# Optimization experiments

Hardware: AMD Instinct MI355X
Metric: run time of the kernel (lower is better)

Reference implementation:

```python
import jax, jax.numpy as jnp
import numpy as np

GROUPS = 32
EPS = 1e-5


def _group_norm(x, scale, bias):
    B, C, H, W = x.shape
    xg = x.reshape(B, GROUPS, -1)
    mu = xg.mean(axis=-1, keepdims=True)
    var = jnp.mean(jnp.square(xg - mu), axis=-1, keepdims=True)
    xn = ((xg - mu) * jax.lax.rsqrt(var + EPS)).reshape(B, C, H, W)
    return xn * scale[None, :, None, None] + bias[None, :, None, None]


def _conv1x1(x, w, b):
    # x: [B,C,H,W], w: [O,C], b: [O]
    return jnp.einsum('bchw,oc->bohw', x, w) + b[None, :, None, None]


def setup_inputs() -> dict:
    key = jax.random.key(0)
    ks = jax.random.split(key, 6)
    B, C, H, W = 16, 512, 32, 32
    x = jax.random.normal(ks[0], (B, C, H, W), dtype=jnp.float32)
    # xavier_uniform for [C, C, 1, 1] conv: limit = sqrt(6 / (fan_in + fan_out)) = sqrt(6 / (2C))
    lim = float(np.sqrt(6.0 / (2 * C)))
    wq = jax.random.uniform(ks[1], (C, C), jnp.float32, -lim, lim)
    wk = jax.random.uniform(ks[2], (C, C), jnp.float32, -lim, lim)
    wv = jax.random.uniform(ks[3], (C, C), jnp.float32, -lim, lim)
    wo = jax.random.uniform(ks[4], (C, C), jnp.float32, -lim, lim) * 1e-5  # gain=1e-5
    zeros_c = jnp.zeros((C,), jnp.float32)
    return {
        'x': x,
        'gn_scale': jnp.ones((C,), jnp.float32),
        'gn_bias': zeros_c,
        'wq': wq, 'bq': zeros_c,
        'wk': wk, 'bk': zeros_c,
        'wv': wv, 'bv': zeros_c,
        'wo': wo, 'bo': zeros_c,
    }


def reference(x, gn_scale, gn_bias, wq, bq, wk, bk, wv, bv, wo, bo):
    B, C, H, W = x.shape
    N = H * W
    h = _group_norm(x, gn_scale, gn_bias)
    q = _conv1x1(h, wq, bq).reshape(B, C, N)  # [B,C,N]
    k = _conv1x1(h, wk, bk).reshape(B, C, N)
    v = _conv1x1(h, wv, bv).reshape(B, C, N)
    scale = 1.0 / jnp.sqrt(jnp.asarray(C, x.dtype))
    w = jnp.einsum('bcn,bcm->bnm', q, k) * scale  # [B,N,N]
    w = jax.nn.softmax(w, axis=-1)
    hv = jnp.einsum('bnm,bcm->bcn', w, v).reshape(B, C, H, W)
    out = _conv1x1(hv, wo, bo)
    return x + out
```

## Files before the change

kernel.cpp:

```cpp
#include <hip/hip_runtime.h>
#include <hip/hip_bf16.h>
#include <cstdint>

typedef unsigned char u8;
typedef float floatx4 __attribute__((ext_vector_type(4)));
typedef int intx8 __attribute__((ext_vector_type(8)));

__device__ __forceinline__ void gld_lds16(const void* g, void* l) {
    __builtin_amdgcn_global_load_lds(
        (const __attribute__((address_space(1))) unsigned int*)g,
        (__attribute__((address_space(3))) unsigned int*)l, 16, 0, 0);
}

__device__ __forceinline__ u8 f2fp8(float v) {
    return (u8)(__builtin_amdgcn_cvt_pk_fp8_f32(v, v, 0, false) & 0xff);
}
__device__ __forceinline__ unsigned int pack4_fp8(float a, float b, float c, float d) {
    unsigned int u = __builtin_amdgcn_cvt_pk_fp8_f32(a, b, 0, false);
    u = __builtin_amdgcn_cvt_pk_fp8_f32(c, d, u, true);
    return u;
}

__device__ __forceinline__ intx8 ld_frag(const u8* p, int lo, int hi) {
    uint4 a = *(const uint4*)(p + lo);
    uint4 b = *(const uint4*)(p + hi);
    intx8 r;
    r[0] = a.x; r[1] = a.y; r[2] = a.z; r[3] = a.w;
    r[4] = b.x; r[5] = b.y; r[6] = b.z; r[7] = b.w;
    return r;
}
__device__ __forceinline__ intx8 ld_frag_g(const u8* p) {
    uint4 a = *(const uint4*)(p);
    uint4 b = *(const uint4*)(p + 16);
    intx8 r;
    r[0] = a.x; r[1] = a.y; r[2] = a.z; r[3] = a.w;
    r[4] = b.x; r[5] = b.y; r[6] = b.z; r[7] = b.w;
    return r;
}


__global__ __launch_bounds__(256) void setup_kernel(
    const float* __restrict__ x, const float* __restrict__ gs,
    const float* __restrict__ gb,
    const float* __restrict__ wq, const float* __restrict__ wk,
    const float* __restrict__ wv, const float* __restrict__ wo,
    const float* __restrict__ bq, const float* __restrict__ bk,
    const float* __restrict__ bv,
    u8* __restrict__ hT, u8* __restrict__ wqkv, u8* __restrict__ wob,
    float* __restrict__ bqkv)
{
    const int t = threadIdx.x;
    if (blockIdx.x >= 512) {
        int i = (blockIdx.x - 512) * 256 + t;
        if (i < 786432) {
            int which = i >> 18;
            int off = i & 262143;
            const float* src = which == 0 ? wq : which == 1 ? wk : wv;
            wqkv[i] = f2fp8(src[off]);
        } else {
            int i2 = i - 786432;
            int row = i2 >> 9, col = i2 & 511;
            wob[(long long)(row >> 4) * 8192 + (col >> 5) * 512
                + (row & 15) * 32 + (col & 31)] = f2fp8(wo[i2] * 262144.0f);
        }
        if (i < 1536)
            bqkv[i] = i < 512 ? bq[i] : (i < 1024 ? bk[i - 512] : bv[i - 1024]);
        return;
    }
    const int b = blockIdx.x >> 5;
    const int g = blockIdx.x & 31;
    const int wave = t >> 6, lane = t & 63;
    const float4* x4 = (const float4*)(x + ((long long)b * 512 + g * 16) * 1024);

    float4 v[16];
    float s1 = 0.f, s2 = 0.f;
#pragma unroll
    for (int i = 0; i < 16; ++i) {
        v[i] = x4[i * 256 + t];
        s1 += v[i].x + v[i].y + v[i].z + v[i].w;
        s2 += v[i].x * v[i].x + v[i].y * v[i].y + v[i].z * v[i].z + v[i].w * v[i].w;
    }
#pragma unroll
    for (int m = 32; m; m >>= 1) {
        s1 += __shfl_xor(s1, m, 64);
        s2 += __shfl_xor(s2, m, 64);
    }
    __shared__ float red[2][4];
    __shared__ float stats[2];
    if (lane == 0) { red[0][wave] = s1; red[1][wave] = s2; }
    __syncthreads();
    if (t == 0) {
        float a = red[0][0] + red[0][1] + red[0][2] + red[0][3];
        float q = red[1][0] + red[1][1] + red[1][2] + red[1][3];
        float mu = a * (1.0f / 16384.0f);
        float var = q * (1.0f / 16384.0f) - mu * mu;
        stats[0] = mu;
        stats[1] = rsqrtf(var + 1e-5f);
    }
    __syncthreads();
    const float mu = stats[0], rs = stats[1];

#pragma unroll
    for (int i = 0; i < 16; ++i) {
        const float sc = gs[g * 16 + i] * rs;
        const float bi = gb[g * 16 + i] - mu * sc;
        v[i].x = v[i].x * sc + bi;
        v[i].y = v[i].y * sc + bi;
        v[i].z = v[i].z * sc + bi;
        v[i].w = v[i].w * sc + bi;
    }
    u8* hb = hT + (long long)b * 524288 + g * 16;
#pragma unroll
    for (int r = 0; r < 4; ++r) {
        uint4 o;
        o.x = pack4_fp8(v[0][r],  v[1][r],  v[2][r],  v[3][r]);
        o.y = pack4_fp8(v[4][r],  v[5][r],  v[6][r],  v[7][r]);
        o.z = pack4_fp8(v[8][r],  v[9][r],  v[10][r], v[11][r]);
        o.w = pack4_fp8(v[12][r], v[13][r], v[14][r], v[15][r]);
        *(uint4*)(hb + (long long)(4 * t + r) * 512) = o;
    }
}

template <int EPI>
__global__ __launch_bounds__(256, 3) void gemm_mx(
    const u8* __restrict__ A, long long sA,
    const u8* __restrict__ B, long long sB,
    void* __restrict__ C, long long sC,
    void* __restrict__ C2, void* __restrict__ C3,
    int ldC, int K,
    const float* __restrict__ bias)
{
    __shared__ __align__(16) u8 smem[33792];
    const int tid = threadIdx.x;
    const int l = tid & 63;
    const int wave = tid >> 6;
    const int wm = wave >> 1, wn = wave & 1;
    const int bm = blockIdx.x, bn = blockIdx.y, b = blockIdx.z;

    const u8* Ab = A + (long long)b * sA + (long long)bm * 128 * K;
    const u8* Bb = B + (long long)b * sB + (long long)bn * 128 * K;

    const int srow = wave * 8 + (l >> 3);
    const int sg = ((l & 7) ^ ((l >> 3) & 7)) * 16;
    const u8* ga  = Ab + (long long)srow * K + sg;
    const u8* gbp = Bb + (long long)srow * K + sg;
    const long long c32 = (long long)32 * K;
    const int ldst = wave * 1024;

    const int q4 = l >> 4;
    const int ln = l & 15;
    const int glo = ((2 * q4) ^ (l & 7)) * 16;
    const int ghi = ((2 * q4 + 1) ^ (l & 7)) * 16;
    int arow[4], brow[4];
#pragma unroll
    for (int i = 0; i < 4; ++i) {
        arow[i] = (wm * 64 + i * 16 + ln) * 128;
        brow[i] = (wn * 64 + i * 16 + ln) * 128 + 16384;
    }

    floatx4 acc[4][4] = {};
    const int niter = K >> 7;

    for (int it = 0; it < niter; ++it) {
        const int k0 = it << 7;
#pragma unroll
        for (int c = 0; c < 4; ++c) {
            gld_lds16(ga + c * c32 + k0, smem + c * 4096 + ldst);
            gld_lds16(gbp + c * c32 + k0, smem + 16384 + c * 4096 + ldst);
        }
        __syncthreads();
        intx8 bfr[4];
#pragma unroll
        for (int j = 0; j < 4; ++j) bfr[j] = ld_frag(smem + brow[j], glo, ghi);
#pragma unroll
        for (int i = 0; i < 4; ++i) {
            intx8 af = ld_frag(smem + arow[i], glo, ghi);
#pragma unroll
            for (int j = 0; j < 4; ++j)
                acc[i][j] = __builtin_amdgcn_mfma_scale_f32_16x16x128_f8f6f4(
                    af, bfr[j], acc[i][j], 0, 0, 0, 127, 0, 127);
        }
        __syncthreads();
    }

    {
        const int which = bn >> 2;
        u8* tile = smem;
#pragma unroll
        for (int i = 0; i < 4; ++i) {
            const int rl = wm * 64 + i * 16 + q4 * 4;
#pragma unroll
            for (int j = 0; j < 4; ++j) {
                const int cl = wn * 64 + j * 16 + ln;
                const float badd = bias[bn * 128 + cl];
                if (which == 2) {
                    *(unsigned int*)(tile + cl * 144 + rl) =
                        pack4_fp8(acc[i][j][0] + badd, acc[i][j][1] + badd,
                                  acc[i][j][2] + badd, acc[i][j][3] + badd);
                } else {
#pragma unroll
                    for (int r = 0; r < 4; ++r)
                        tile[(rl + r) * 144 + cl] = f2fp8(acc[i][j][r] + badd);
                }
            }
        }
        __syncthreads();
        const int w2  = wave >> 1;
        const int cbl = (wave & 1) * 2 + (l >> 5);
        const int lnw = (l >> 1) & 15;
        const int g16 = (l & 1) * 16;
#pragma unroll
        for (int p = 0; p < 4; ++p) {
            const int rtile = p * 2 + w2;
            uint4 dd = *(const uint4*)(tile + (rtile * 16 + lnw) * 144 + cbl * 32 + g16);
            u8* dst;
            if (which == 0)
                dst = (u8*)C + (long long)b * sC + (long long)(bm * 8 + rtile) * 8192
                      + ((bn & 3) * 4 + cbl) * 512 + lnw * 32 + g16;
            else if (which == 1)
                dst = (u8*)C2 + (long long)b * sC + (long long)(bm * 8 + rtile) * 8192
                      + ((bn & 3) * 4 + cbl) * 512 + lnw * 32 + g16;
            else
                dst = (u8*)C3 + (long long)b * sC + (long long)((bn & 3) * 8 + rtile) * 16384
                      + (long long)(bm * 4 + cbl) * 512 + lnw * 32 + g16;
            *(uint4*)dst = dd;
        }
    }
}

__global__ __launch_bounds__(256, 2) void attn_out(
    const u8* __restrict__ qg, const u8* __restrict__ kg,
    const u8* __restrict__ vg, const u8* __restrict__ wot,
    const float* __restrict__ bo, const float* __restrict__ xg,
    float* __restrict__ outg)
{
    __shared__ __align__(16) u8 smem[25088];
    const int tid = threadIdx.x;
    const int l = tid & 63;
    const int w = tid >> 6;
    const int d = blockIdx.x;
    const int b  = (d & 7) * 2 + ((d >> 8) & 1);
    const int bq = (d >> 3) & 31;

    const u8* qb = qg + (long long)b * 524288 + (long long)(bq * 2) * 8192;
    const u8* kb = kg + (long long)b * 524288;
    const u8* vb = vg + (long long)b * 524288;

    const int q4 = l >> 4;
    const int ln = l & 15;
    const int glo = ((2 * q4) ^ (l & 7)) * 16;
    const int ghi = ((2 * q4 + 1) ^ (l & 7)) * 16;
    const int lo32 = ln * 32;

    intx8 qf[2][4];
#pragma unroll
    for (int j = 0; j < 2; ++j)
#pragma unroll
        for (int kc = 0; kc < 4; ++kc)
            qf[j][kc] = ld_frag_g(qb + j * 8192 + (kc * 4 + q4) * 512 + lo32);

    intx8 kreg[2][4];
#pragma unroll
    for (int i = 0; i < 2; ++i)
#pragma unroll
        for (int kc = 0; kc < 4; ++kc)
            kreg[i][kc] = ld_frag_g(kb + (long long)(w * 2 + i) * 8192
                                       + (kc * 4 + q4) * 512 + lo32);

    floatx4 acc_pv[8][2] = {};
    float psum[2] = {0.f, 0.f};
    const float scale = 0.044194173824159216f;

    for (int mt = 0; mt < 8; ++mt) {
        u8* E = smem + (mt & 1) * 4096;
        floatx4 acc_s[2][2] = {};
#pragma unroll
        for (int kc = 0; kc < 4; ++kc)
#pragma unroll
            for (int i = 0; i < 2; ++i)
#pragma unroll
                for (int j = 0; j < 2; ++j)
                    acc_s[i][j] = __builtin_amdgcn_mfma_scale_f32_16x16x128_f8f6f4(
                        kreg[i][kc], qf[j][kc], acc_s[i][j], 0, 0, 0, 127, 0, 127);
        intx8 vfA[4], vfB[4];
        const u8* vrow = vb + (long long)(w * 8) * 16384 + (mt * 4 + q4) * 512 + lo32;
#pragma unroll
        for (int i = 0; i < 4; ++i)
            vfA[i] = ld_frag_g(vrow + (long long)i * 16384);
#pragma unroll
        for (int i = 0; i < 2; ++i) {
#pragma unroll
            for (int j = 0; j < 2; ++j) {
                float e0 = __expf(acc_s[i][j][0] * scale);
                float e1 = __expf(acc_s[i][j][1] * scale);
                float e2 = __expf(acc_s[i][j][2] * scale);
                float e3 = __expf(acc_s[i][j][3] * scale);
                psum[j] += e0 + e1 + e2 + e3;
                const int n = j * 16 + ln;
                const int m0 = w * 32 + i * 16 + q4 * 4;
                *(unsigned int*)(E + n * 128 + (m0 ^ ((n & 7) * 16))) =
                    pack4_fp8(e0 * 0.25f, e1 * 0.25f, e2 * 0.25f, e3 * 0.25f);
            }
        }
        __syncthreads();
        if (mt < 7) {
            const u8* kn = kb + (long long)((mt + 1) * 8 + w * 2) * 8192
                              + q4 * 512 + lo32;
#pragma unroll
            for (int i = 0; i < 2; ++i)
#pragma unroll
                for (int kc = 0; kc < 4; ++kc)
                    kreg[i][kc] = ld_frag_g(kn + (long long)i * 8192 + kc * 2048);
        }
#pragma unroll
        for (int i = 0; i < 4; ++i)
            vfB[i] = ld_frag_g(vrow + (long long)(i + 4) * 16384);
        intx8 ef[2];
#pragma unroll
        for (int j = 0; j < 2; ++j)
            ef[j] = ld_frag(E + (j * 16 + ln) * 128, glo, ghi);
#pragma unroll
        for (int i = 0; i < 4; ++i)
#pragma unroll
            for (int j = 0; j < 2; ++j)
                acc_pv[i][j] = __builtin_amdgcn_mfma_scale_f32_16x16x128_f8f6f4(
                    vfA[i], ef[j], acc_pv[i][j], 0, 0, 0, 127, 0, 127);
#pragma unroll
        for (int i = 0; i < 4; ++i)
#pragma unroll
            for (int j = 0; j < 2; ++j)
                acc_pv[i + 4][j] = __builtin_amdgcn_mfma_scale_f32_16x16x128_f8f6f4(
                    vfB[i], ef[j], acc_pv[i + 4][j], 0, 0, 0, 127, 0, 127);
    }

#pragma unroll
    for (int j = 0; j < 2; ++j) {
        psum[j] += __shfl_xor(psum[j], 16, 64);
        psum[j] += __shfl_xor(psum[j], 32, 64);
    }
    float* sb = (float*)(smem + 8192);
    if (l < 16) {
        sb[w * 32 + l]      = psum[0];
        sb[w * 32 + 16 + l] = psum[1];
    }
    __syncthreads();
    float rln[2];
#pragma unroll
    for (int j = 0; j < 2; ++j) {
        const int n = j * 16 + ln;
        rln[j] = 4.0f / (sb[n] + sb[32 + n] + sb[64 + n] + sb[96 + n]);
    }

    u8* HV = smem + 8704;
#pragma unroll
    for (int i = 0; i < 8; ++i) {
#pragma unroll
        for (int j = 0; j < 2; ++j) {
            const int n = j * 16 + ln;
            const int m0 = i * 16 + q4 * 4;
            *(unsigned int*)(HV + w * 4096 + n * 128 + (m0 ^ ((n & 7) * 16))) =
                pack4_fp8(acc_pv[i][j][0] * rln[j], acc_pv[i][j][1] * rln[j],
                          acc_pv[i][j][2] * rln[j], acc_pv[i][j][3] * rln[j]);
        }
    }
    intx8 wo0[2];
#pragma unroll
    for (int rb = 0; rb < 2; ++rb)
        wo0[rb] = ld_frag_g(wot + (long long)(w * 8 + rb) * 8192 + q4 * 512 + lo32);
    __syncthreads();

    floatx4 acc2[8][2] = {};
#pragma unroll
    for (int kc = 0; kc < 4; ++kc) {
        intx8 hvf[2];
#pragma unroll
        for (int j = 0; j < 2; ++j)
            hvf[j] = ld_frag(HV + kc * 4096 + (j * 16 + ln) * 128, glo, ghi);
#pragma unroll
        for (int rb = 0; rb < 8; ++rb) {
            intx8 wof = (kc == 0 && rb < 2) ? wo0[rb]
                : ld_frag_g(wot + (long long)(w * 8 + rb) * 8192
                                + (kc * 4 + q4) * 512 + lo32);
#pragma unroll
            for (int j = 0; j < 2; ++j)
                acc2[rb][j] = __builtin_amdgcn_mfma_scale_f32_16x16x128_f8f6f4(
                    wof, hvf[j], acc2[rb][j], 0, 0, 0, 127, 0, 127);
        }
    }

    const float osc = 3.814697265625e-06f;
    const float* xb = xg + (long long)b * 524288;
    float* og = outg + (long long)b * 524288;
    const int n0 = bq * 32;
#pragma unroll
    for (int rb = 0; rb < 8; ++rb) {
        const int oc0 = w * 128 + rb * 16 + q4 * 4;
#pragma unroll
        for (int j = 0; j < 2; ++j) {
            const int n = n0 + j * 16 + ln;
#pragma unroll
            for (int r = 0; r < 4; ++r) {
                const int oc = oc0 + r;
                og[(long long)oc * 1024 + n] =
                    acc2[rb][j][r] * osc + bo[oc] + xb[(long long)oc * 1024 + n];
            }
        }
    }
}

extern "C" void kernel_launch(void* const* d_in, const int* in_sizes, int n_in,
                              void* d_out, int out_size, void* d_ws, size_t ws_size,
                              hipStream_t stream)
{
    const float* x  = (const float*)d_in[0];
    const float* gs = (const float*)d_in[1];
    const float* gb = (const float*)d_in[2];
    const float* wq = (const float*)d_in[3];
    const float* bq = (const float*)d_in[4];
    const float* wk = (const float*)d_in[5];
    const float* bk = (const float*)d_in[6];
    const float* wv = (const float*)d_in[7];
    const float* bv = (const float*)d_in[8];
    const float* wo = (const float*)d_in[9];
    const float* bo = (const float*)d_in[10];
    float* out = (float*)d_out;

    u8* p = (u8*)d_ws;
    u8* hT   = p; p += 8388608;
    u8* q    = p; p += 8388608;
    u8* k    = p; p += 8388608;
    u8* v    = p; p += 8388608;
    u8* wqkv = p; p += 786432;
    float* bqkv = (float*)p; p += 6144;
    u8* wob  = p; p += 262144;

    setup_kernel<<<4608, 256, 0, stream>>>(x, gs, gb, wq, wk, wv, wo, bq, bk, bv,
                                           hT, wqkv, wob, bqkv);

    gemm_mx<1><<<dim3(8, 12, 16), 256, 0, stream>>>(
        hT, 524288LL, wqkv, 0LL, q, 524288LL, k, v,
        512, 512, bqkv);

    attn_out<<<dim3(512, 1, 1), 256, 0, stream>>>(q, k, v, wob, bo, x, out);
}
```

Measured before the change: 166.0 us.

## Pre-fragment normalized activations and load QKV GEMM A operand directly from global

The group-norm kernel now writes hT in an MFMA-fragment-tiled layout, so the QKV GEMM can load A fragments straight from global memory into registers instead of staging them through LDS. The whole 128x512 B weight tile is loaded into a 64KB LDS buffer once, with a single barrier in place of a per-K-step barrier loop. Launch bounds drop to one block per SM for both the GEMM and attn_out. In exchange, the larger LDS footprint lowers occupancy, and the scattered global fragment loads could expose latency.

```diff
diff --git a/kernel.cpp b/kernel.cpp
--- a/kernel.cpp
+++ b/kernel.cpp
@@ -109,79 +109,77 @@
         v[i].z = v[i].z * sc + bi;
         v[i].w = v[i].w * sc + bi;
     }
-    u8* hb = hT + (long long)b * 524288 + g * 16;
+    u8* hb = hT + (long long)b * 524288 + (g >> 1) * 512 + (g & 1) * 16;
 #pragma unroll
     for (int r = 0; r < 4; ++r) {
+        const int pos = 4 * t + r;
         uint4 o;
         o.x = pack4_fp8(v[0][r],  v[1][r],  v[2][r],  v[3][r]);
         o.y = pack4_fp8(v[4][r],  v[5][r],  v[6][r],  v[7][r]);
         o.z = pack4_fp8(v[8][r],  v[9][r],  v[10][r], v[11][r]);
         o.w = pack4_fp8(v[12][r], v[13][r], v[14][r], v[15][r]);
-        *(uint4*)(hb + (long long)(4 * t + r) * 512) = o;
-    }
-}
-
-template <int EPI>
-__global__ __launch_bounds__(256, 3) void gemm_mx(
-    const u8* __restrict__ A, long long sA,
-    const u8* __restrict__ B, long long sB,
-    void* __restrict__ C, long long sC,
-    void* __restrict__ C2, void* __restrict__ C3,
-    int ldC, int K,
+        *(uint4*)(hb + (long long)(pos >> 4) * 8192 + (pos & 15) * 32) = o;
+    }
+}
+
+__global__ __launch_bounds__(256, 1) void gemm_qkv(
+    const u8* __restrict__ A,
+    const u8* __restrict__ B,
+    u8* __restrict__ Cq, u8* __restrict__ Ck, u8* __restrict__ Cv,
     const float* __restrict__ bias)
 {
-    __shared__ __align__(16) u8 smem[33792];
+    __shared__ __align__(16) u8 smem[65536];
     const int tid = threadIdx.x;
     const int l = tid & 63;
     const int wave = tid >> 6;
     const int wm = wave >> 1, wn = wave & 1;
     const int bm = blockIdx.x, bn = blockIdx.y, b = blockIdx.z;
 
-    const u8* Ab = A + (long long)b * sA + (long long)bm * 128 * K;
-    const u8* Bb = B + (long long)b * sB + (long long)bn * 128 * K;
-
-    const int srow = wave * 8 + (l >> 3);
-    const int sg = ((l & 7) ^ ((l >> 3) & 7)) * 16;
-    const u8* ga  = Ab + (long long)srow * K + sg;
-    const u8* gbp = Bb + (long long)srow * K + sg;
-    const long long c32 = (long long)32 * K;
-    const int ldst = wave * 1024;
-
     const int q4 = l >> 4;
     const int ln = l & 15;
     const int glo = ((2 * q4) ^ (l & 7)) * 16;
     const int ghi = ((2 * q4 + 1) ^ (l & 7)) * 16;
-    int arow[4], brow[4];
-#pragma unroll
-    for (int i = 0; i < 4; ++i) {
-        arow[i] = (wm * 64 + i * 16 + ln) * 128;
-        brow[i] = (wn * 64 + i * 16 + ln) * 128 + 16384;
-    }
+    const int lo32 = ln * 32;
+
+    const int srow = wave * 8 + (l >> 3);
+    const int sg = ((l & 7) ^ ((l >> 3) & 7)) * 16;
+    const u8* Bb = B + (long long)bn * 128 * 512;
+    const int ldst = wave * 1024;
+#pragma unroll
+    for (int kc = 0; kc < 4; ++kc)
+#pragma unroll
+        for (int rc = 0; rc < 4; ++rc)
+            gld_lds16(Bb + (long long)(rc * 32 + srow) * 512 + kc * 128 + sg,
+                      smem + kc * 16384 + rc * 4096 + ldst);
+
+    const u8* Ab = A + (long long)b * 524288 + (long long)(bm * 8 + wm * 4) * 8192;
+    intx8 af0[4];
+#pragma unroll
+    for (int i = 0; i < 4; ++i)
+        af0[i] = ld_frag_g(Ab + (long long)i * 8192 + q4 * 512 + lo32);
+
+    __syncthreads();
 
     floatx4 acc[4][4] = {};
-    const int niter = K >> 7;
-
-    for (int it = 0; it < niter; ++it) {
-        const int k0 = it << 7;
-#pragma unroll
-        for (int c = 0; c < 4; ++c) {
-            gld_lds16(ga + c * c32 + k0, smem + c * 4096 + ldst);
-            gld_lds16(gbp + c * c32 + k0, smem + 16384 + c * 4096 + ldst);
-        }
-        __syncthreads();
+#pragma unroll
+    for (int kc = 0; kc < 4; ++kc) {
         intx8 bfr[4];
 #pragma unroll
-        for (int j = 0; j < 4; ++j) bfr[j] = ld_frag(smem + brow[j], glo, ghi);
+        for (int j = 0; j < 4; ++j)
+            bfr[j] = ld_frag(smem + kc * 16384 + (wn * 64 + j * 16 + ln) * 128,
+                             glo, ghi);
 #pragma unroll
         for (int i = 0; i < 4; ++i) {
-            intx8 af = ld_frag(smem + arow[i], glo, ghi);
+            intx8 af = (kc == 0) ? af0[i]
+                : ld_frag_g(Ab + (long long)i * 8192 + (kc * 4 + q4) * 512 + lo32);
 #pragma unroll
             for (int j = 0; j < 4; ++j)
                 acc[i][j] = __builtin_amdgcn_mfma_scale_f32_16x16x128_f8f6f4(
                     af, bfr[j], acc[i][j], 0, 0, 0, 127, 0, 127);
         }
-        __syncthreads();
-    }
+    }
+
+    __syncthreads();
 
     {
         const int which = bn >> 2;
@@ -215,20 +213,20 @@
             uint4 dd = *(const uint4*)(tile + (rtile * 16 + lnw) * 144 + cbl * 32 + g16);
             u8* dst;
             if (which == 0)
-                dst = (u8*)C + (long long)b * sC + (long long)(bm * 8 + rtile) * 8192
+                dst = Cq + (long long)b * 524288 + (long long)(bm * 8 + rtile) * 8192
                       + ((bn & 3) * 4 + cbl) * 512 + lnw * 32 + g16;
             else if (which == 1)
-                dst = (u8*)C2 + (long long)b * sC + (long long)(bm * 8 + rtile) * 8192
+                dst = Ck + (long long)b * 524288 + (long long)(bm * 8 + rtile) * 8192
                       + ((bn & 3) * 4 + cbl) * 512 + lnw * 32 + g16;
             else
-                dst = (u8*)C3 + (long long)b * sC + (long long)((bn & 3) * 8 + rtile) * 16384
+                dst = Cv + (long long)b * 524288 + (long long)((bn & 3) * 8 + rtile) * 16384
                       + (long long)(bm * 4 + cbl) * 512 + lnw * 32 + g16;
             *(uint4*)dst = dd;
         }
     }
 }
 
-__global__ __launch_bounds__(256, 2) void attn_out(
+__global__ __launch_bounds__(256, 1) void attn_out(
     const u8* __restrict__ qg, const u8* __restrict__ kg,
     const u8* __restrict__ vg, const u8* __restrict__ wot,
     const float* __restrict__ bo, const float* __restrict__ xg,
@@ -437,9 +435,7 @@
     setup_kernel<<<4608, 256, 0, stream>>>(x, gs, gb, wq, wk, wv, wo, bq, bk, bv,
                                            hT, wqkv, wob, bqkv);
 
-    gemm_mx<1><<<dim3(8, 12, 16), 256, 0, stream>>>(
-        hT, 524288LL, wqkv, 0LL, q, 524288LL, k, v,
-        512, 512, bqkv);
+    gemm_qkv<<<dim3(8, 12, 16), 256, 0, stream>>>(hT, wqkv, q, k, v, bqkv);
 
     attn_out<<<dim3(512, 1, 1), 256, 0, stream>>>(q, k, v, wob, bo, x, out);
 }
```

Result: slower. 172.5 us (+3.9%).
